# Performance work log

Hardware: AMD Instinct MI355X
Metric: run time of the kernel (lower is better)

## Reference

```python
import jax, jax.numpy as jnp
import numpy as np

ALPHA = 0.2
SIGMA_REC = 0.15


def setup_inputs() -> dict:
    key = jax.random.key(0)
    k1, k2, k3, k4 = jax.random.split(key, 4)
    B, T, IN, N = 512, 1024, 6, 64
    u = jax.random.normal(k1, (B, T, IN), dtype=jnp.float32)
    noise = jax.random.normal(k2, (B, T, N), dtype=jnp.float32)
    W_rec = jax.random.normal(k3, (N, N), dtype=jnp.float32) / N
    W_in = (1.0 / np.sqrt(N)) * (1.0 + jax.random.normal(k4, (N, IN), dtype=jnp.float32))
    return {"u": u, "noise": noise, "W_rec": W_rec, "W_in": W_in}


def reference(u, noise, W_rec, W_in):
    # u: [B, T, in], noise: [B, T, n] (standard normal), W_rec: [n, n], W_in: [n, in]
    B, T, _ = u.shape
    n = W_rec.shape[0]
    scale = jnp.sqrt(2.0 * ALPHA * SIGMA_REC ** 2).astype(u.dtype)
    noise_s = scale * noise

    def step(s, inp):
        ui, ni = inp  # [B, in], [B, n]
        pre = s @ W_rec.T + ui @ W_in.T + ni
        s_new = (1.0 - ALPHA) * s + ALPHA * jax.nn.relu(pre)
        return s_new, s_new

    s0 = jnp.zeros((B, n), dtype=u.dtype)
    # loop runs t-1 steps (uses u[:, :T-1], noise[:, :T-1]); states[:,0]=0
    xs = (jnp.swapaxes(u[:, :-1], 0, 1), jnp.swapaxes(noise_s[:, :-1], 0, 1))
    _, ys = jax.lax.scan(step, s0, xs)  # ys: [T-1, B, n]
    states = jnp.concatenate([s0[:, None, :], jnp.swapaxes(ys, 0, 1)], axis=1)  # [B, T, n]
    return states
```

## Files before the change

### kernel.cpp

```cpp
#include <hip/hip_runtime.h>

typedef float v2f __attribute__((ext_vector_type(2)));
typedef float v4f __attribute__((ext_vector_type(4)));

#define TT 1024
#define NIN 6
#define NN 64
#define CHUNK 32
#define NCHUNK 32
#define SCALE 0.09486832980505137f

__device__ __forceinline__ v2f pk_fma(v2f a, v2f b, v2f c) {
  return __builtin_elementwise_fma(a, b, c);
}

typedef const __attribute__((address_space(1))) unsigned int gu32;
typedef __attribute__((address_space(3))) unsigned int lu32;

__global__ void __launch_bounds__(64) rnn_scan_kernel(
    const float* __restrict__ u, const float* __restrict__ noise,
    const float* __restrict__ Wrec, const float* __restrict__ Win,
    float* __restrict__ out) {
  const int b = blockIdx.x;
  const int n = threadIdx.x;

  __shared__ __align__(16) float smHist[CHUNK][NN];
  __shared__ __align__(16) float smNz[2][CHUNK * NN];
  __shared__ __align__(16) float smU[2][CHUNK * NIN];

  const float* nzg = noise + (size_t)b * TT * NN;
  const float* ug  = u + (size_t)b * TT * NIN;
  float* outB = out + (size_t)b * TT * NN;

#pragma unroll
  for (int i = 0; i < 8; ++i)
    __builtin_amdgcn_global_load_lds((gu32*)(nzg + i * 256 + n * 4),
                                     (lu32*)(&smNz[0][i * 256]), 16, 0, 0);
#pragma unroll
  for (int j = 0; j < 3; ++j)
    __builtin_amdgcn_global_load_lds((gu32*)(ug + j * 64 + n),
                                     (lu32*)(&smU[0][j * 64]), 4, 0, 0);

  v2f w2[NN / 2];
#pragma unroll
  for (int k = 0; k < NN; k += 4) {
    const float4 v = *reinterpret_cast<const float4*>(Wrec + n * NN + k);
    w2[k / 2 + 0] = v2f{v.x, v.y};
    w2[k / 2 + 1] = v2f{v.z, v.w};
  }
  v2f win2[3];
#pragma unroll
  for (int j = 0; j < 3; ++j)
    win2[j] = v2f{Win[n * NIN + 2 * j + 0], Win[n * NIN + 2 * j + 1]};

  float s = 0.0f;
  smHist[CHUNK - 1][n] = 0.0f;
  outB[n] = 0.0f;

  asm volatile("s_waitcnt vmcnt(0)" ::: "memory");
  __builtin_amdgcn_sched_barrier(0);

  for (int c = 0; c < NCHUNK; ++c) {
    const int buf = c & 1;

    if (c + 1 < NCHUNK) {
      const float* ng = nzg + (size_t)(c + 1) * CHUNK * NN;
      const float* gg = ug + (size_t)(c + 1) * CHUNK * NIN;
      float* nl = &smNz[buf ^ 1][0];
      float* ul = &smU[buf ^ 1][0];
#pragma unroll
      for (int i = 0; i < 8; ++i)
        __builtin_amdgcn_global_load_lds((gu32*)(ng + i * 256 + n * 4),
                                         (lu32*)(nl + i * 256), 16, 0, 0);
#pragma unroll
      for (int j = 0; j < 3; ++j)
        __builtin_amdgcn_global_load_lds((gu32*)(gg + j * 64 + n),
                                         (lu32*)(ul + j * 64), 4, 0, 0);
      asm volatile("s_waitcnt vmcnt(19)" ::: "memory");
    } else {
      asm volatile("s_waitcnt vmcnt(8)" ::: "memory");
    }
    __builtin_amdgcn_sched_barrier(0);

    const float* nzL = &smNz[buf][0] + n;
    const float* uL  = &smU[buf][0];

#pragma unroll 4
    for (int st = 0; st < CHUNK; ++st) {
      const int prev = (st + CHUNK - 1) & (CHUNK - 1);
      const float nzc = nzL[st * NN];
      const v2f* u2 = (const v2f*)(uL + st * NIN);
      v2f a0 = v2f{SCALE * nzc, 0.0f};
      v2f a1 = v2f{0.0f, 0.0f}, a2 = v2f{0.0f, 0.0f}, a3 = v2f{0.0f, 0.0f};
      a0 = pk_fma(u2[0], win2[0], a0);
      a1 = pk_fma(u2[1], win2[1], a1);
      a2 = pk_fma(u2[2], win2[2], a2);
      const v4f* sv = (const v4f*)(&smHist[prev][0]);
#pragma unroll
      for (int q = 0; q < 16; q += 2) {
        const v4f qa = sv[q + 0];
        a0 = pk_fma(v2f{qa.x, qa.y}, w2[2 * q + 0], a0);
        a1 = pk_fma(v2f{qa.z, qa.w}, w2[2 * q + 1], a1);
        const v4f qb = sv[q + 1];
        a2 = pk_fma(v2f{qb.x, qb.y}, w2[2 * q + 2], a2);
        a3 = pk_fma(v2f{qb.z, qb.w}, w2[2 * q + 3], a3);
      }
      const v2f at = (a0 + a1) + (a2 + a3);
      const float pre = at.x + at.y;
      const float r = fmaxf(pre, 0.0f);
      s = fmaf(0.2f, r, 0.8f * s);
      smHist[st][n] = s;
    }

    v4f st4[8];
    const float* hbase = &smHist[0][0] + (n >> 4) * NN + (n & 15) * 4;
#pragma unroll
    for (int i = 0; i < 8; ++i)
      st4[i] = *(const v4f*)(hbase + i * 4 * NN);

    float* gp = outB + (size_t)(c * CHUNK + 1) * NN + (n >> 4) * NN + (n & 15) * 4;
    if (c + 1 < NCHUNK) {
#pragma unroll
      for (int i = 0; i < 8; ++i)
        *(v4f*)(gp + (size_t)i * 4 * NN) = st4[i];
    } else {
#pragma unroll
      for (int i = 0; i < 7; ++i)
        *(v4f*)(gp + (size_t)i * 4 * NN) = st4[i];
      if (n < 48)
        *(v4f*)(gp + (size_t)7 * 4 * NN) = st4[7];
    }
  }
}

extern "C" void kernel_launch(void* const* d_in, const int* in_sizes, int n_in,
                              void* d_out, int out_size, void* d_ws, size_t ws_size,
                              hipStream_t stream) {
  const float* u     = (const float*)d_in[0];
  const float* noise = (const float*)d_in[1];
  const float* Wrec  = (const float*)d_in[2];
  const float* Win   = (const float*)d_in[3];
  float* out = (float*)d_out;

  const int B = in_sizes[0] / (TT * NIN);
  hipLaunchKernelGGL(rnn_scan_kernel, dim3(B), dim3(64), 0, stream,
                     u, noise, Wrec, Win, out);
}
```

Before: 208.7 us.

## Broadcast packed fp16 state via readlane and use fdot2 for recurrence

Replaces the per-step LDS reads of the previous hidden state with a cross-lane broadcast. Each lane packs its own state and its neighbour's (obtained with DPP) into an fp16 pair, and the 32 pairs are fetched with readlane into scalar registers. The recurrent matvec then uses fp16 dot2 instructions against W_rec converted to fp16. The aim is to remove LDS latency and halve the FMA count on the serial critical path, at the cost of reduced precision in the recurrence and in the weights. That precision loss may accumulate over 1023 steps and break tolerance.

```diff
diff --git a/kernel.cpp b/kernel.cpp
--- a/kernel.cpp
+++ b/kernel.cpp
@@ -2,6 +2,7 @@
 
 typedef float v2f __attribute__((ext_vector_type(2)));
 typedef float v4f __attribute__((ext_vector_type(4)));
+typedef __fp16 v2h __attribute__((ext_vector_type(2)));
 
 #define TT 1024
 #define NIN 6
@@ -12,6 +13,13 @@
 
 __device__ __forceinline__ v2f pk_fma(v2f a, v2f b, v2f c) {
   return __builtin_elementwise_fma(a, b, c);
+}
+
+__device__ __forceinline__ v2h h2_from_i(int i) {
+  return __builtin_bit_cast(v2h, i);
+}
+__device__ __forceinline__ int i_from_h2(v2h h) {
+  return __builtin_bit_cast(int, h);
 }
 
 typedef const __attribute__((address_space(1))) unsigned int gu32;
@@ -41,12 +49,12 @@
     __builtin_amdgcn_global_load_lds((gu32*)(ug + j * 64 + n),
                                      (lu32*)(&smU[0][j * 64]), 4, 0, 0);
 
-  v2f w2[NN / 2];
+  v2h w16[NN / 2];
 #pragma unroll
   for (int k = 0; k < NN; k += 4) {
     const float4 v = *reinterpret_cast<const float4*>(Wrec + n * NN + k);
-    w2[k / 2 + 0] = v2f{v.x, v.y};
-    w2[k / 2 + 1] = v2f{v.z, v.w};
+    w16[k / 2 + 0] = __builtin_amdgcn_cvt_pkrtz(v.x, v.y);
+    w16[k / 2 + 1] = __builtin_amdgcn_cvt_pkrtz(v.z, v.w);
   }
   v2f win2[3];
 #pragma unroll
@@ -54,6 +62,7 @@
     win2[j] = v2f{Win[n * NIN + 2 * j + 0], Win[n * NIN + 2 * j + 1]};
 
   float s = 0.0f;
+  int hpk = 0;
   smHist[CHUNK - 1][n] = 0.0f;
   outB[n] = 0.0f;
 
@@ -87,29 +96,60 @@
 
 #pragma unroll 4
     for (int st = 0; st < CHUNK; ++st) {
-      const int prev = (st + CHUNK - 1) & (CHUNK - 1);
       const float nzc = nzL[st * NN];
-      const v2f* u2 = (const v2f*)(uL + st * NIN);
-      v2f a0 = v2f{SCALE * nzc, 0.0f};
-      v2f a1 = v2f{0.0f, 0.0f}, a2 = v2f{0.0f, 0.0f}, a3 = v2f{0.0f, 0.0f};
-      a0 = pk_fma(u2[0], win2[0], a0);
-      a1 = pk_fma(u2[1], win2[1], a1);
-      a2 = pk_fma(u2[2], win2[2], a2);
-      const v4f* sv = (const v4f*)(&smHist[prev][0]);
+      const v2f* u2p = (const v2f*)(uL + st * NIN);
+      v2f uacc = pk_fma(u2p[0], win2[0], v2f{SCALE * nzc, 0.0f});
+      uacc = pk_fma(u2p[1], win2[1], uacc);
+      uacc = pk_fma(u2p[2], win2[2], uacc);
+
+      float a0, a1, a2, a3, a4, a5, a6, a7;
+      {
+        int r0 = __builtin_amdgcn_readlane(hpk, 0);
+        int r1 = __builtin_amdgcn_readlane(hpk, 2);
+        int r2 = __builtin_amdgcn_readlane(hpk, 4);
+        int r3 = __builtin_amdgcn_readlane(hpk, 6);
+        int r4 = __builtin_amdgcn_readlane(hpk, 8);
+        int r5 = __builtin_amdgcn_readlane(hpk, 10);
+        int r6 = __builtin_amdgcn_readlane(hpk, 12);
+        int r7 = __builtin_amdgcn_readlane(hpk, 14);
+        a0 = __builtin_amdgcn_fdot2(h2_from_i(r0), w16[0], 0.0f, false);
+        a1 = __builtin_amdgcn_fdot2(h2_from_i(r1), w16[1], 0.0f, false);
+        a2 = __builtin_amdgcn_fdot2(h2_from_i(r2), w16[2], 0.0f, false);
+        a3 = __builtin_amdgcn_fdot2(h2_from_i(r3), w16[3], 0.0f, false);
+        a4 = __builtin_amdgcn_fdot2(h2_from_i(r4), w16[4], 0.0f, false);
+        a5 = __builtin_amdgcn_fdot2(h2_from_i(r5), w16[5], 0.0f, false);
+        a6 = __builtin_amdgcn_fdot2(h2_from_i(r6), w16[6], 0.0f, false);
+        a7 = __builtin_amdgcn_fdot2(h2_from_i(r7), w16[7], 0.0f, false);
+      }
 #pragma unroll
-      for (int q = 0; q < 16; q += 2) {
-        const v4f qa = sv[q + 0];
-        a0 = pk_fma(v2f{qa.x, qa.y}, w2[2 * q + 0], a0);
-        a1 = pk_fma(v2f{qa.z, qa.w}, w2[2 * q + 1], a1);
-        const v4f qb = sv[q + 1];
-        a2 = pk_fma(v2f{qb.x, qb.y}, w2[2 * q + 2], a2);
-        a3 = pk_fma(v2f{qb.z, qb.w}, w2[2 * q + 3], a3);
+      for (int j = 1; j < 4; ++j) {
+        int r0 = __builtin_amdgcn_readlane(hpk, 16 * j + 0);
+        int r1 = __builtin_amdgcn_readlane(hpk, 16 * j + 2);
+        int r2 = __builtin_amdgcn_readlane(hpk, 16 * j + 4);
+        int r3 = __builtin_amdgcn_readlane(hpk, 16 * j + 6);
+        int r4 = __builtin_amdgcn_readlane(hpk, 16 * j + 8);
+        int r5 = __builtin_amdgcn_readlane(hpk, 16 * j + 10);
+        int r6 = __builtin_amdgcn_readlane(hpk, 16 * j + 12);
+        int r7 = __builtin_amdgcn_readlane(hpk, 16 * j + 14);
+        a0 = __builtin_amdgcn_fdot2(h2_from_i(r0), w16[8 * j + 0], a0, false);
+        a1 = __builtin_amdgcn_fdot2(h2_from_i(r1), w16[8 * j + 1], a1, false);
+        a2 = __builtin_amdgcn_fdot2(h2_from_i(r2), w16[8 * j + 2], a2, false);
+        a3 = __builtin_amdgcn_fdot2(h2_from_i(r3), w16[8 * j + 3], a3, false);
+        a4 = __builtin_amdgcn_fdot2(h2_from_i(r4), w16[8 * j + 4], a4, false);
+        a5 = __builtin_amdgcn_fdot2(h2_from_i(r5), w16[8 * j + 5], a5, false);
+        a6 = __builtin_amdgcn_fdot2(h2_from_i(r6), w16[8 * j + 6], a6, false);
+        a7 = __builtin_amdgcn_fdot2(h2_from_i(r7), w16[8 * j + 7], a7, false);
       }
-      const v2f at = (a0 + a1) + (a2 + a3);
-      const float pre = at.x + at.y;
+
+      float pre = ((a0 + a1) + (a2 + a3)) + ((a4 + a5) + (a6 + a7));
+      pre += uacc.x + uacc.y;
       const float r = fmaxf(pre, 0.0f);
       s = fmaf(0.2f, r, 0.8f * s);
       smHist[st][n] = s;
+
+      const int part = __builtin_amdgcn_update_dpp(
+          0, __float_as_int(s), 0xB1 , 0xF, 0xF, false);
+      hpk = i_from_h2(__builtin_amdgcn_cvt_pkrtz(s, __int_as_float(part)));
     }
 
     v4f st4[8];
```

Result: slower. 229.4 us (+9.9%).

## Broadcast state via DPP/permlane swaps and use fp16 dot2 for recurrence

Applied to the files above, without the earlier changes.

Replaces the per-step LDS round trip for the previous hidden state with an in-register all-gather across the wavefront, built from DPP moves and permlane16/32 swaps on fp16-packed pairs. The recurrent matvec then runs with fdot2 on half-precision weight pairs, permuted at setup to match the gather order. The aim is to remove LDS read latency and the barrier-like dependency from the serial recurrence. It lowers precision of the state and weights to fp16 with round-toward-zero conversion, which may cause error to build up over 1023 steps.

```diff
diff --git a/kernel.cpp b/kernel.cpp
--- a/kernel.cpp
+++ b/kernel.cpp
@@ -2,6 +2,7 @@
 
 typedef float v2f __attribute__((ext_vector_type(2)));
 typedef float v4f __attribute__((ext_vector_type(4)));
+typedef __fp16 v2h __attribute__((ext_vector_type(2)));
 
 #define TT 1024
 #define NIN 6
@@ -12,6 +13,36 @@
 
 __device__ __forceinline__ v2f pk_fma(v2f a, v2f b, v2f c) {
   return __builtin_elementwise_fma(a, b, c);
+}
+__device__ __forceinline__ v2h h2_from_i(int i) { return __builtin_bit_cast(v2h, i); }
+__device__ __forceinline__ int i_from_h2(v2h h) { return __builtin_bit_cast(int, h); }
+
+template <int CTRL>
+__device__ __forceinline__ int dppmov(int src) {
+  return __builtin_amdgcn_update_dpp(0, src, CTRL, 0xF, 0xF, true);
+}
+
+__device__ __forceinline__ void gather64(float v, int g[32]) {
+  const int part = dppmov<0xB1>(__float_as_int(v));
+  const int p0 = i_from_h2(__builtin_amdgcn_cvt_pkrtz(v, __int_as_float(part)));
+  g[0] = p0;
+  g[1] = dppmov<0x4E>(p0);
+  g[2] = dppmov<0x124>(g[0]);
+  g[3] = dppmov<0x124>(g[1]);
+  g[4] = dppmov<0x128>(g[0]);
+  g[5] = dppmov<0x128>(g[1]);
+  g[6] = dppmov<0x128>(g[2]);
+  g[7] = dppmov<0x128>(g[3]);
+#pragma unroll
+  for (int i = 0; i < 8; ++i) {
+    auto r = __builtin_amdgcn_permlane16_swap(g[i], g[i], false, false);
+    g[i] = r[0]; g[8 + i] = r[1];
+  }
+#pragma unroll
+  for (int i = 0; i < 16; ++i) {
+    auto r = __builtin_amdgcn_permlane32_swap(g[i], g[i], false, false);
+    g[i] = r[0]; g[16 + i] = r[1];
+  }
 }
 
 typedef const __attribute__((address_space(1))) unsigned int gu32;
@@ -41,12 +72,16 @@
     __builtin_amdgcn_global_load_lds((gu32*)(ug + j * 64 + n),
                                      (lu32*)(&smU[0][j * 64]), 4, 0, 0);
 
-  v2f w2[NN / 2];
+  int gidx[32];
+  gather64((float)n, gidx);
+  v2h w16[32];
+  const float* wrow = Wrec + n * NN;
 #pragma unroll
-  for (int k = 0; k < NN; k += 4) {
-    const float4 v = *reinterpret_cast<const float4*>(Wrec + n * NN + k);
-    w2[k / 2 + 0] = v2f{v.x, v.y};
-    w2[k / 2 + 1] = v2f{v.z, v.w};
+  for (int j = 0; j < 32; ++j) {
+    const v2h ij = h2_from_i(gidx[j]);
+    const int k0 = (int)(float)ij[0];
+    const int k1 = (int)(float)ij[1];
+    w16[j] = __builtin_amdgcn_cvt_pkrtz(wrow[k0], wrow[k1]);
   }
   v2f win2[3];
 #pragma unroll
@@ -54,7 +89,6 @@
     win2[j] = v2f{Win[n * NIN + 2 * j + 0], Win[n * NIN + 2 * j + 1]};
 
   float s = 0.0f;
-  smHist[CHUNK - 1][n] = 0.0f;
   outB[n] = 0.0f;
 
   asm volatile("s_waitcnt vmcnt(0)" ::: "memory");
@@ -87,26 +121,26 @@
 
 #pragma unroll 4
     for (int st = 0; st < CHUNK; ++st) {
-      const int prev = (st + CHUNK - 1) & (CHUNK - 1);
       const float nzc = nzL[st * NN];
-      const v2f* u2 = (const v2f*)(uL + st * NIN);
-      v2f a0 = v2f{SCALE * nzc, 0.0f};
-      v2f a1 = v2f{0.0f, 0.0f}, a2 = v2f{0.0f, 0.0f}, a3 = v2f{0.0f, 0.0f};
-      a0 = pk_fma(u2[0], win2[0], a0);
-      a1 = pk_fma(u2[1], win2[1], a1);
-      a2 = pk_fma(u2[2], win2[2], a2);
-      const v4f* sv = (const v4f*)(&smHist[prev][0]);
+      const v2f* u2p = (const v2f*)(uL + st * NIN);
+      v2f uacc = pk_fma(u2p[0], win2[0], v2f{SCALE * nzc, 0.0f});
+      uacc = pk_fma(u2p[1], win2[1], uacc);
+      uacc = pk_fma(u2p[2], win2[2], uacc);
+
+      int g[32];
+      gather64(s, g);
+      float acc[8];
 #pragma unroll
-      for (int q = 0; q < 16; q += 2) {
-        const v4f qa = sv[q + 0];
-        a0 = pk_fma(v2f{qa.x, qa.y}, w2[2 * q + 0], a0);
-        a1 = pk_fma(v2f{qa.z, qa.w}, w2[2 * q + 1], a1);
-        const v4f qb = sv[q + 1];
-        a2 = pk_fma(v2f{qb.x, qb.y}, w2[2 * q + 2], a2);
-        a3 = pk_fma(v2f{qb.z, qb.w}, w2[2 * q + 3], a3);
-      }
-      const v2f at = (a0 + a1) + (a2 + a3);
-      const float pre = at.x + at.y;
+      for (int j = 0; j < 8; ++j)
+        acc[j] = __builtin_amdgcn_fdot2(h2_from_i(g[j]), w16[j], 0.0f, false);
+#pragma unroll
+      for (int j = 8; j < 32; ++j)
+        acc[j & 7] =
+            __builtin_amdgcn_fdot2(h2_from_i(g[j]), w16[j], acc[j & 7], false);
+
+      float pre = ((acc[0] + acc[1]) + (acc[2] + acc[3])) +
+                  ((acc[4] + acc[5]) + (acc[6] + acc[7]));
+      pre += uacc.x + uacc.y;
       const float r = fmaxf(pre, 0.0f);
       s = fmaf(0.2f, r, 0.8f * s);
       smHist[st][n] = s;
```

Measured after the change: 306.3 us. 46.8% more time.

## Split recurrent matvec across lane quads with fp16 dot2 and DPP reduction

Applied to the files above, without the earlier changes.

Each lane now computes partial dot products for 4 output neurons over a 16-element slice of the state, using packed fp16 weights and v_dot2 instructions. Partials are combined with DPP quad reductions, and the new state is redistributed through ds_bpermute rather than read back from LDS each step. The aim is to cut per-step FMA count and LDS read traffic on the serial critical path. In exchange, the recurrent state and weights go through fp16 rounding, which may accumulate error over 1023 steps, and each step gains cross-lane permute latency.

```diff
diff --git a/kernel.cpp b/kernel.cpp
--- a/kernel.cpp
+++ b/kernel.cpp
@@ -2,6 +2,7 @@
 
 typedef float v2f __attribute__((ext_vector_type(2)));
 typedef float v4f __attribute__((ext_vector_type(4)));
+typedef __fp16 v2h __attribute__((ext_vector_type(2)));
 
 #define TT 1024
 #define NIN 6
@@ -10,8 +11,13 @@
 #define NCHUNK 32
 #define SCALE 0.09486832980505137f
 
-__device__ __forceinline__ v2f pk_fma(v2f a, v2f b, v2f c) {
-  return __builtin_elementwise_fma(a, b, c);
+__device__ __forceinline__ v2h h2_from_i(int i) { return __builtin_bit_cast(v2h, i); }
+__device__ __forceinline__ int i_from_h2(v2h h) { return __builtin_bit_cast(int, h); }
+
+template <int CTRL>
+__device__ __forceinline__ float dppf(float x) {
+  return __int_as_float(
+      __builtin_amdgcn_update_dpp(0, __float_as_int(x), CTRL, 0xF, 0xF, true));
 }
 
 typedef const __attribute__((address_space(1))) unsigned int gu32;
@@ -22,7 +28,9 @@
     const float* __restrict__ Wrec, const float* __restrict__ Win,
     float* __restrict__ out) {
   const int b = blockIdx.x;
-  const int n = threadIdx.x;
+  const int l = threadIdx.x;
+  const int g = l >> 2;
+  const int h = l & 3;
 
   __shared__ __align__(16) float smHist[CHUNK][NN];
   __shared__ __align__(16) float smNz[2][CHUNK * NN];
@@ -34,28 +42,44 @@
 
 #pragma unroll
   for (int i = 0; i < 8; ++i)
-    __builtin_amdgcn_global_load_lds((gu32*)(nzg + i * 256 + n * 4),
+    __builtin_amdgcn_global_load_lds((gu32*)(nzg + i * 256 + l * 4),
                                      (lu32*)(&smNz[0][i * 256]), 16, 0, 0);
 #pragma unroll
   for (int j = 0; j < 3; ++j)
-    __builtin_amdgcn_global_load_lds((gu32*)(ug + j * 64 + n),
+    __builtin_amdgcn_global_load_lds((gu32*)(ug + j * 64 + l),
                                      (lu32*)(&smU[0][j * 64]), 4, 0, 0);
 
-  v2f w2[NN / 2];
+  v2h w16[4][8];
 #pragma unroll
-  for (int k = 0; k < NN; k += 4) {
-    const float4 v = *reinterpret_cast<const float4*>(Wrec + n * NN + k);
-    w2[k / 2 + 0] = v2f{v.x, v.y};
-    w2[k / 2 + 1] = v2f{v.z, v.w};
+  for (int r = 0; r < 4; ++r) {
+    const float* row = Wrec + (4 * g + r) * NN + 16 * h;
+#pragma unroll
+    for (int j4 = 0; j4 < 4; ++j4) {
+      const v4f v = *reinterpret_cast<const v4f*>(row + 4 * j4);
+      w16[r][2 * j4 + 0] = __builtin_amdgcn_cvt_pkrtz(v.x, v.y);
+      w16[r][2 * j4 + 1] = __builtin_amdgcn_cvt_pkrtz(v.z, v.w);
+    }
   }
-  v2f win2[3];
+  const int hh = (h < 3) ? h : 0;
+  v2h winu[4];
 #pragma unroll
-  for (int j = 0; j < 3; ++j)
-    win2[j] = v2f{Win[n * NIN + 2 * j + 0], Win[n * NIN + 2 * j + 1]};
+  for (int r = 0; r < 4; ++r) {
+    const float a0 = Win[(4 * g + r) * NIN + 2 * hh + 0];
+    const float a1 = Win[(4 * g + r) * NIN + 2 * hh + 1];
+    const v2h wp = __builtin_amdgcn_cvt_pkrtz(a0, a1);
+    winu[r] = (h < 3) ? wp : v2h{(__fp16)0.0f, (__fp16)0.0f};
+  }
 
-  float s = 0.0f;
-  smHist[CHUNK - 1][n] = 0.0f;
-  outB[n] = 0.0f;
+  int baddr[4];
+#pragma unroll
+  for (int q = 0; q < 4; ++q) baddr[q] = 4 * (16 * h + 4 * q + (g & 3));
+
+  float sOut[4] = {0.0f, 0.0f, 0.0f, 0.0f};
+  int sK[8];
+#pragma unroll
+  for (int j = 0; j < 8; ++j) sK[j] = 0;
+
+  outB[l] = 0.0f;
 
   asm volatile("s_waitcnt vmcnt(0)" ::: "memory");
   __builtin_amdgcn_sched_barrier(0);
@@ -70,11 +94,11 @@
       float* ul = &smU[buf ^ 1][0];
 #pragma unroll
       for (int i = 0; i < 8; ++i)
-        __builtin_amdgcn_global_load_lds((gu32*)(ng + i * 256 + n * 4),
+        __builtin_amdgcn_global_load_lds((gu32*)(ng + i * 256 + l * 4),
                                          (lu32*)(nl + i * 256), 16, 0, 0);
 #pragma unroll
       for (int j = 0; j < 3; ++j)
-        __builtin_amdgcn_global_load_lds((gu32*)(gg + j * 64 + n),
+        __builtin_amdgcn_global_load_lds((gu32*)(gg + j * 64 + l),
                                          (lu32*)(ul + j * 64), 4, 0, 0);
       asm volatile("s_waitcnt vmcnt(19)" ::: "memory");
     } else {
@@ -82,43 +106,62 @@
     }
     __builtin_amdgcn_sched_barrier(0);
 
-    const float* nzL = &smNz[buf][0] + n;
-    const float* uL  = &smU[buf][0];
+    const float* nzB = &smNz[buf][4 * g];
+    const float* uB  = &smU[buf][2 * hh];
 
 #pragma unroll 4
     for (int st = 0; st < CHUNK; ++st) {
-      const int prev = (st + CHUNK - 1) & (CHUNK - 1);
-      const float nzc = nzL[st * NN];
-      const v2f* u2 = (const v2f*)(uL + st * NIN);
-      v2f a0 = v2f{SCALE * nzc, 0.0f};
-      v2f a1 = v2f{0.0f, 0.0f}, a2 = v2f{0.0f, 0.0f}, a3 = v2f{0.0f, 0.0f};
-      a0 = pk_fma(u2[0], win2[0], a0);
-      a1 = pk_fma(u2[1], win2[1], a1);
-      a2 = pk_fma(u2[2], win2[2], a2);
-      const v4f* sv = (const v4f*)(&smHist[prev][0]);
+      const v4f nz4 = *reinterpret_cast<const v4f*>(nzB + st * NN);
+      const v2f u2  = *reinterpret_cast<const v2f*>(uB + st * NIN);
+      const v2h u2h = __builtin_amdgcn_cvt_pkrtz(u2.x, u2.y);
+      float partial[4];
 #pragma unroll
-      for (int q = 0; q < 16; q += 2) {
-        const v4f qa = sv[q + 0];
-        a0 = pk_fma(v2f{qa.x, qa.y}, w2[2 * q + 0], a0);
-        a1 = pk_fma(v2f{qa.z, qa.w}, w2[2 * q + 1], a1);
-        const v4f qb = sv[q + 1];
-        a2 = pk_fma(v2f{qb.x, qb.y}, w2[2 * q + 2], a2);
-        a3 = pk_fma(v2f{qb.z, qb.w}, w2[2 * q + 3], a3);
+      for (int r = 0; r < 4; ++r) {
+        const float nb = (h == 3) ? SCALE * nz4[r] : 0.0f;
+        partial[r] = __builtin_amdgcn_fdot2(u2h, winu[r], nb, false);
       }
-      const v2f at = (a0 + a1) + (a2 + a3);
-      const float pre = at.x + at.y;
-      const float r = fmaxf(pre, 0.0f);
-      s = fmaf(0.2f, r, 0.8f * s);
-      smHist[st][n] = s;
+
+#pragma unroll
+      for (int j = 0; j < 8; ++j) {
+        const v2h sj = h2_from_i(sK[j]);
+#pragma unroll
+        for (int r = 0; r < 4; ++r)
+          partial[r] = __builtin_amdgcn_fdot2(sj, w16[r][j], partial[r], false);
+      }
+
+#pragma unroll
+      for (int r = 0; r < 4; ++r) partial[r] += dppf<0xB1>(partial[r]);
+#pragma unroll
+      for (int r = 0; r < 4; ++r) partial[r] += dppf<0x4E>(partial[r]);
+
+#pragma unroll
+      for (int r = 0; r < 4; ++r) {
+        const float rr = fmaxf(partial[r], 0.0f);
+        sOut[r] = fmaf(0.2f, rr, 0.8f * sOut[r]);
+      }
+
+      {
+        const float va = (h & 1) ? sOut[1] : sOut[0];
+        const float vb = (h & 1) ? sOut[3] : sOut[2];
+        smHist[st][l] = (h & 2) ? vb : va;
+      }
+
+      const int pk01 = i_from_h2(__builtin_amdgcn_cvt_pkrtz(sOut[0], sOut[1]));
+      const int pk23 = i_from_h2(__builtin_amdgcn_cvt_pkrtz(sOut[2], sOut[3]));
+#pragma unroll
+      for (int q = 0; q < 4; ++q) {
+        sK[2 * q + 0] = __builtin_amdgcn_ds_bpermute(baddr[q], pk01);
+        sK[2 * q + 1] = __builtin_amdgcn_ds_bpermute(baddr[q], pk23);
+      }
     }
 
     v4f st4[8];
-    const float* hbase = &smHist[0][0] + (n >> 4) * NN + (n & 15) * 4;
+    const float* hbase = &smHist[0][0] + (l >> 4) * NN + (l & 15) * 4;
 #pragma unroll
     for (int i = 0; i < 8; ++i)
       st4[i] = *(const v4f*)(hbase + i * 4 * NN);
 
-    float* gp = outB + (size_t)(c * CHUNK + 1) * NN + (n >> 4) * NN + (n & 15) * 4;
+    float* gp = outB + (size_t)(c * CHUNK + 1) * NN + (l >> 4) * NN + (l & 15) * 4;
     if (c + 1 < NCHUNK) {
 #pragma unroll
       for (int i = 0; i < 8; ++i)
@@ -127,7 +170,7 @@
 #pragma unroll
       for (int i = 0; i < 7; ++i)
         *(v4f*)(gp + (size_t)i * 4 * NN) = st4[i];
-      if (n < 48)
+      if (l < 48)
         *(v4f*)(gp + (size_t)7 * 4 * NN) = st4[7];
     }
   }
```

New measurement: 239.1 us. 1.15x slower.
